# Kernel tuning notes

Hardware: AMD Instinct MI355X
Metric: run time of the kernel (lower is better)

The kernel has to match this reference:

```python
import jax, jax.numpy as jnp
import numpy as np

HIDDEN = 2048
NUM_HEADS = 16
HEAD_DIM = HIDDEN // NUM_HEADS  # 128
LAYER_IDX = 0


def setup_inputs() -> dict:
    key = jax.random.key(0)
    k1, k2, k3, k4, k5 = jax.random.split(key, 5)
    B, S = 2, 2048
    hidden_states = jax.random.normal(k1, (B, S, HIDDEN), dtype=jnp.float32)
    # causal mask, broadcastable to attn shape (B, Q, H, K)
    causal = jnp.tril(jnp.ones((S, S), dtype=jnp.bool_))  # [Q, K]
    attention_mask = causal[None, :, None, :]  # [1, Q, 1, K]
    c_attn_w = jax.random.normal(k2, (HIDDEN, HIDDEN + 2 * HEAD_DIM), dtype=jnp.float32) * 0.02
    c_attn_b = jax.random.normal(k3, (HIDDEN + 2 * HEAD_DIM,), dtype=jnp.float32) * 0.02
    c_proj_w = jax.random.normal(k4, (HIDDEN, HIDDEN), dtype=jnp.float32) * 0.02
    c_proj_b = jax.random.normal(k5, (HIDDEN,), dtype=jnp.float32) * 0.02
    return {
        "hidden_states": hidden_states,
        "attention_mask": attention_mask,
        "c_attn_w": c_attn_w,
        "c_attn_b": c_attn_b,
        "c_proj_w": c_proj_w,
        "c_proj_b": c_proj_b,
    }


def reference(hidden_states, attention_mask, c_attn_w, c_attn_b, c_proj_w, c_proj_b):
    B, S, D = hidden_states.shape
    H, hd = NUM_HEADS, HEAD_DIM
    # c_attn then split into per-head query and shared (MQA) key/value
    qkv = hidden_states @ c_attn_w + c_attn_b  # [B, S, D + 2*hd]
    query = qkv[..., :D].reshape(B, S, H, hd)  # [B, Q, H, hd]
    k = qkv[..., D:D + hd]                     # [B, K, hd] shared across heads
    v = qkv[..., D + hd:]                      # [B, K, hd]
    # fp32 input => upcast=False => unscale=1, scale = 1/sqrt(head_dim)
    scale = 1.0 / jnp.sqrt(jnp.float32(hd))
    scores = jnp.einsum('bqhd,bkd->bqhk', query, k) * scale  # [B, Q, H, K]
    mask_value = jnp.finfo(jnp.float32).min
    scores = jnp.where(attention_mask, scores, mask_value)
    attn = jax.nn.softmax(scores, axis=-1)
    attn_output = jnp.einsum('bqhk,bkd->bqhd', attn, v).reshape(B, S, D)
    attn_output = attn_output @ c_proj_w + c_proj_b
    return attn_output
```

## Files before the change

kernel.cpp:

```cpp
#include <hip/hip_runtime.h>
#include <hip/hip_bf16.h>

typedef __bf16 bf16_t;
typedef __bf16 bf16x8 __attribute__((ext_vector_type(8)));
typedef __bf16 bf16x4 __attribute__((ext_vector_type(4)));
typedef float f32x4 __attribute__((ext_vector_type(4)));

#define S_LEN 2048
#define HID   2048
#define NH    16
#define HD    128
#define QKVN  2304
#define NEG_BIG (-30000.0f)
#define RESCALE_THR 8.0f

__device__ __forceinline__ void gld_lds16(const bf16_t* g, bf16_t* l) {
  __builtin_amdgcn_global_load_lds(
      (const __attribute__((address_space(1))) void*)((const void*)g),
      (__attribute__((address_space(3))) void*)((void*)l), 16, 0, 0);
}

__global__ __launch_bounds__(256) void cvt_f32_bf16_kernel(
    const float* __restrict__ in, bf16_t* __restrict__ out, int n)
{
  int i = (blockIdx.x * 256 + threadIdx.x) * 4;
  if (i < n) {
    float4 v = *(const float4*)(in + i);
    bf16x4 o;
    o[0] = (bf16_t)v.x; o[1] = (bf16_t)v.y; o[2] = (bf16_t)v.z; o[3] = (bf16_t)v.w;
    *(bf16x4*)(out + i) = o;
  }
}

__global__ __launch_bounds__(256) void transpose_cvt_kernel(
    const float* __restrict__ in, bf16_t* __restrict__ out, int K, int N)
{
  int nc = threadIdx.x & 63;
  int kg = threadIdx.x >> 6;
  int n  = blockIdx.x * 64 + nc;
  int kb = blockIdx.y * 32 + kg * 8;
  bf16x8 v;
  #pragma unroll
  for (int i = 0; i < 8; ++i) v[i] = (bf16_t)in[(size_t)(kb + i) * N + n];
  *(bf16x8*)(out + (size_t)n * K + kb) = v;
}

__global__ __launch_bounds__(256) void vt_extract_kernel(
    const bf16_t* __restrict__ qkv, bf16_t* __restrict__ vtg)
{
  int d  = threadIdx.x & 127;
  int sg = threadIdx.x >> 7;
  int b  = blockIdx.y;
  int s8 = blockIdx.x * 2 + sg;
  bf16x8 v;
  #pragma unroll
  for (int i = 0; i < 8; ++i)
    v[i] = qkv[((size_t)(b * S_LEN + s8 * 8 + i)) * QKVN + HID + HD + d];
  *(bf16x8*)(vtg + ((size_t)(b * HD + d)) * S_LEN + s8 * 8) = v;
}

template <typename OutT>
__global__ __launch_bounds__(256) void gemm_bias_kernel(
    const bf16_t* __restrict__ A, const bf16_t* __restrict__ WT,
    const float* __restrict__ bias, OutT* __restrict__ C,
    int K, int lda, int ldc)
{
  __shared__ bf16_t Ash[128 * 64];
  __shared__ bf16_t Bsh[128 * 64];

  const int tid  = threadIdx.x;
  const int wave = tid >> 6;
  const int lane = tid & 63;
  const int quad = lane >> 4;
  const int c16  = lane & 15;
  const int wm = wave >> 1;
  const int wn = wave & 1;

  int id  = (int)(blockIdx.y * gridDim.x + blockIdx.x);
  int nwg = (int)(gridDim.x * gridDim.y);
  int swz = (nwg & 7) ? id : ((id & 7) * (nwg >> 3) + (id >> 3));
  const int n0 = (swz % (int)gridDim.x) * 128;
  const int m0 = (swz / (int)gridDim.x) * 128;

  f32x4 acc[4][4] = {};

  for (int k0 = 0; k0 < K; k0 += 64) {
    __syncthreads();
    #pragma unroll
    for (int j = 0; j < 4; ++j) {
      int cbase = wave * 256 + j * 64;
      int c = cbase + lane;
      int row = c >> 3;
      int kcl = (c ^ row) & 7;
      gld_lds16(A  + (size_t)(m0 + row) * lda + k0 + kcl * 8, Ash + cbase * 8);
      gld_lds16(WT + (size_t)(n0 + row) * K   + k0 + kcl * 8, Bsh + cbase * 8);
    }
    __syncthreads();

    #pragma unroll
    for (int kk = 0; kk < 2; ++kk) {
      bf16x8 af[4], bfr[4];
      #pragma unroll
      for (int rb = 0; rb < 4; ++rb) {
        int row = wm * 64 + rb * 16 + c16;
        int kcp = ((kk * 4 + quad) ^ row) & 7;
        af[rb] = *(const bf16x8*)(Ash + row * 64 + kcp * 8);
      }
      #pragma unroll
      for (int nt = 0; nt < 4; ++nt) {
        int row = wn * 64 + nt * 16 + c16;
        int kcp = ((kk * 4 + quad) ^ row) & 7;
        bfr[nt] = *(const bf16x8*)(Bsh + row * 64 + kcp * 8);
      }
      #pragma unroll
      for (int rb = 0; rb < 4; ++rb)
        #pragma unroll
        for (int nt = 0; nt < 4; ++nt)
          acc[rb][nt] = __builtin_amdgcn_mfma_f32_16x16x32_bf16(af[rb], bfr[nt],
                                                                acc[rb][nt], 0, 0, 0);
    }
  }

  #pragma unroll
  for (int nt = 0; nt < 4; ++nt) {
    int col = n0 + wn * 64 + nt * 16 + c16;
    float bv = bias[col];
    #pragma unroll
    for (int rb = 0; rb < 4; ++rb) {
      int rbase = m0 + wm * 64 + rb * 16 + quad * 4;
      #pragma unroll
      for (int r = 0; r < 4; ++r)
        C[(size_t)(rbase + r) * ldc + col] = (OutT)(acc[rb][nt][r] + bv);
    }
  }
}

__global__ __launch_bounds__(512, 4) void mqa_attn_kernel(
    const bf16_t* __restrict__ qkv, const bf16_t* __restrict__ vtg,
    bf16_t* __restrict__ out)
{
  __shared__ bf16_t Ksh[2][64 * 136];
  __shared__ bf16_t VTsh[2][128 * 72];

  const int tid  = threadIdx.x;
  const int wave = tid >> 6;
  const int g    = wave >> 2;
  const int wv   = wave & 3;
  const int lane = tid & 63;
  const int quad = lane >> 4;
  const int c16  = lane & 15;
  const int gt   = tid & 255;
  const int h = blockIdx.y;
  const int b = blockIdx.z;
  const float qscale = 0.08838834764831845f * 1.4426950408889634f;

  const bf16_t* kbase = qkv + (size_t)b * S_LEN * QKVN + HID;
  const bf16_t* vtb   = vtg + (size_t)b * HD * S_LEN;

  for (int half = 0; half < 2; ++half) {
    const int qb = half ? (31 - (int)blockIdx.x) : (int)blockIdx.x;
    const int q0 = qb * 64;
    const int qrow = q0 + wv * 16 + c16;

    const bf16_t* qp = qkv + ((size_t)(b * S_LEN + qrow)) * QKVN + h * HD;
    bf16x8 qf[4];
    #pragma unroll
    for (int ks = 0; ks < 4; ++ks) {
      bf16x8 t = *(const bf16x8*)(qp + ks * 32 + quad * 8);
      #pragma unroll
      for (int j = 0; j < 8; ++j) t[j] = (bf16_t)((float)t[j] * qscale);
      qf[ks] = t;
    }

    float m_q = NEG_BIG, l_q = 0.0f;
    f32x4 o[8] = {};
    const int nss = (qb + 2) >> 1;

    for (int ss = 0; ss < nss; ++ss) {
      const int kt = 2 * ss + g;
      const bool active = (kt <= qb);

      __syncthreads();
      if (active) {
        for (int c = gt; c < 1024; c += 256) {
          int key = c >> 4, dc = c & 15;
          *(bf16x8*)(&Ksh[g][key * 136 + dc * 8]) =
              *(const bf16x8*)(kbase + (size_t)(kt * 64 + key) * QKVN + dc * 8);
        }
        for (int c = gt; c < 1024; c += 256) {
          int d = c >> 3, kc = c & 7;
          *(bf16x8*)(&VTsh[g][d * 72 + kc * 8]) =
              *(const bf16x8*)(vtb + (size_t)d * S_LEN + kt * 64 + kc * 8);
        }
      }
      __syncthreads();

      float p[4][4];
      if (active) {
        f32x4 sacc[4] = {};
        __builtin_amdgcn_s_setprio(1);
        #pragma unroll
        for (int mt = 0; mt < 4; ++mt) {
          #pragma unroll
          for (int ks = 0; ks < 4; ++ks) {
            bf16x8 kf = *(const bf16x8*)(&Ksh[g][(mt * 16 + c16) * 136 + ks * 32 + quad * 8]);
            sacc[mt] = __builtin_amdgcn_mfma_f32_16x16x32_bf16(kf, qf[ks], sacc[mt], 0, 0, 0);
          }
        }
        __builtin_amdgcn_s_setprio(0);
        float mx = NEG_BIG;
        if (kt == qb) {
          #pragma unroll
          for (int mt = 0; mt < 4; ++mt) {
            #pragma unroll
            for (int r = 0; r < 4; ++r) {
              int key = kt * 64 + mt * 16 + quad * 4 + r;
              float v = sacc[mt][r];
              if (key > qrow) v = NEG_BIG;
              p[mt][r] = v;
              mx = fmaxf(mx, v);
            }
          }
        } else {
          #pragma unroll
          for (int mt = 0; mt < 4; ++mt) {
            #pragma unroll
            for (int r = 0; r < 4; ++r) {
              p[mt][r] = sacc[mt][r];
              mx = fmaxf(mx, sacc[mt][r]);
            }
          }
        }
        mx = fmaxf(mx, __shfl_xor(mx, 16));
        mx = fmaxf(mx, __shfl_xor(mx, 32));

        if (__any(mx > m_q + RESCALE_THR)) {
          float mn = fmaxf(m_q, mx);
          float alpha = __builtin_exp2f(m_q - mn);
          m_q = mn;
          l_q *= alpha;
          #pragma unroll
          for (int mt8 = 0; mt8 < 8; ++mt8) {
            #pragma unroll
            for (int r = 0; r < 4; ++r) o[mt8][r] *= alpha;
          }
        }

        float rs = 0.f;
        #pragma unroll
        for (int mt = 0; mt < 4; ++mt) {
          #pragma unroll
          for (int r = 0; r < 4; ++r) {
            float pe = __builtin_exp2f(p[mt][r] - m_q);
            p[mt][r] = pe;
            rs += pe;
          }
        }
        rs += __shfl_xor(rs, 16);
        rs += __shfl_xor(rs, 32);
        l_q += rs;
      }

      __syncthreads();
      if (active) {
        bf16_t* Pw = &Ksh[g][(wv * 16) * 136];
        #pragma unroll
        for (int mt = 0; mt < 4; ++mt) {
          bf16x4 pk;
          #pragma unroll
          for (int r = 0; r < 4; ++r) pk[r] = (bf16_t)p[mt][r];
          *(bf16x4*)(Pw + c16 * 136 + mt * 16 + quad * 4) = pk;
        }
        bf16x8 pf[2];
        #pragma unroll
        for (int kh = 0; kh < 2; ++kh)
          pf[kh] = *(const bf16x8*)(Pw + c16 * 136 + kh * 32 + quad * 8);
        __builtin_amdgcn_s_setprio(1);
        #pragma unroll
        for (int mt8 = 0; mt8 < 8; ++mt8) {
          #pragma unroll
          for (int kh = 0; kh < 2; ++kh) {
            bf16x8 vf = *(const bf16x8*)(&VTsh[g][(mt8 * 16 + c16) * 72 + kh * 32 + quad * 8]);
            o[mt8] = __builtin_amdgcn_mfma_f32_16x16x32_bf16(vf, pf[kh], o[mt8], 0, 0, 0);
          }
        }
        __builtin_amdgcn_s_setprio(0);
      }
    }

    __syncthreads();
    float* scr = (float*)&VTsh[0][0];
    float* mls = scr + 4 * 16 * 132;
    if (g == 1) {
      float* op = scr + (wv * 16 + c16) * 132;
      #pragma unroll
      for (int mt8 = 0; mt8 < 8; ++mt8)
        *(f32x4*)(op + mt8 * 16 + quad * 4) = o[mt8];
      if (quad == 0) {
        mls[wv * 32 + c16] = m_q;
        mls[wv * 32 + 16 + c16] = l_q;
      }
    }
    __syncthreads();
    if (g == 0) {
      float m1 = mls[wv * 32 + c16];
      float l1 = mls[wv * 32 + 16 + c16];
      float mF = fmaxf(m_q, m1);
      float a0 = __builtin_exp2f(m_q - mF);
      float a1 = __builtin_exp2f(m1 - mF);
      float inv = 1.0f / fmaxf(a0 * l_q + a1 * l1, 1e-20f);
      a0 *= inv; a1 *= inv;
      const float* op = scr + (wv * 16 + c16) * 132;
      bf16_t* Osh = &Ksh[0][(wv * 16) * 136];
      #pragma unroll
      for (int mt8 = 0; mt8 < 8; ++mt8) {
        f32x4 o1 = *(const f32x4*)(op + mt8 * 16 + quad * 4);
        bf16x4 pk;
        #pragma unroll
        for (int r = 0; r < 4; ++r) pk[r] = (bf16_t)(o[mt8][r] * a0 + o1[r] * a1);
        *(bf16x4*)(Osh + c16 * 136 + mt8 * 16 + quad * 4) = pk;
      }
      int ql = lane >> 2, dc = lane & 3;
      #pragma unroll
      for (int i = 0; i < 4; ++i) {
        bf16x8 v = *(const bf16x8*)(Osh + ql * 136 + dc * 8 + i * 32);
        *(bf16x8*)(out + ((size_t)(b * S_LEN + q0 + wv * 16 + ql)) * HID
                       + h * HD + dc * 8 + i * 32) = v;
      }
    }
  }
}

extern "C" void kernel_launch(void* const* d_in, const int* in_sizes, int n_in,
                              void* d_out, int out_size, void* d_ws, size_t ws_size,
                              hipStream_t stream) {
  const float* hidden_f   = (const float*)d_in[0];
  const float* c_attn_w_f = (const float*)d_in[2];
  const float* c_attn_b_f = (const float*)d_in[3];
  const float* c_proj_w_f = (const float*)d_in[4];
  const float* c_proj_b_f = (const float*)d_in[5];
  float* out = (float*)d_out;

  const int M = 2 * S_LEN;
  const int nH  = M * HID;
  const int nWq = HID * QKVN;
  const int nWp = HID * HID;

  bf16_t* hbf   = (bf16_t*)d_ws;
  bf16_t* wqT   = hbf  + nH;
  bf16_t* wpT   = wqT  + nWq;
  bf16_t* qkv   = wpT  + nWp;
  bf16_t* attn  = qkv  + (size_t)M * QKVN;
  bf16_t* vtg   = attn + (size_t)M * HID;

  cvt_f32_bf16_kernel<<<nH / 1024, 256, 0, stream>>>(hidden_f, hbf, nH);
  dim3 gt1(QKVN / 64, HID / 32);
  transpose_cvt_kernel<<<gt1, 256, 0, stream>>>(c_attn_w_f, wqT, HID, QKVN);
  dim3 gt2(HID / 64, HID / 32);
  transpose_cvt_kernel<<<gt2, 256, 0, stream>>>(c_proj_w_f, wpT, HID, HID);

  dim3 g1(QKVN / 128, M / 128);
  gemm_bias_kernel<bf16_t><<<g1, 256, 0, stream>>>(hbf, wqT, c_attn_b_f, qkv,
                                                   HID, HID, QKVN);

  dim3 gv(S_LEN / 16, 2);
  vt_extract_kernel<<<gv, 256, 0, stream>>>(qkv, vtg);

  dim3 g2(16, NH, 2);
  mqa_attn_kernel<<<g2, 512, 0, stream>>>(qkv, vtg, attn);

  dim3 g3(HID / 128, M / 128);
  gemm_bias_kernel<float><<<g3, 256, 0, stream>>>(attn, wpT, c_proj_b_f, out,
                                                  HID, HID, HID);
}
```

Measured before the change: 338.0 us.

## Restructure MQA attention to 128-row query tiles with swizzled P buffer

The attention kernel now gives each block one 128-row query tile, with each of the 8 waves owning 16 rows. This replaces the old scheme of two wave groups splitting KV tiles and merging partial softmax states at the end. Each K/V tile loaded into LDS is shared by twice as many queries, which removes the cross-group merge and one set of shared buffers. The P staging area uses an XOR swizzle to cut LDS bank conflicts, and the query-block mapping is rotated by head and batch to balance causal work across blocks. Waves whose rows lie entirely before a KV tile skip compute, but they still hit every barrier.

```diff
diff --git a/kernel.cpp b/kernel.cpp
--- a/kernel.cpp
+++ b/kernel.cpp
@@ -139,17 +139,15 @@
     const bf16_t* __restrict__ qkv, const bf16_t* __restrict__ vtg,
     bf16_t* __restrict__ out)
 {
-  __shared__ bf16_t Ksh[2][64 * 136];
-  __shared__ bf16_t VTsh[2][128 * 72];
+  __shared__ bf16_t sh[17920];
+  bf16_t* Ksh  = sh;
+  bf16_t* VTsh = sh + 64 * 136;
 
   const int tid  = threadIdx.x;
-  const int wave = tid >> 6;
-  const int g    = wave >> 2;
-  const int wv   = wave & 3;
+  const int wv   = tid >> 6;
   const int lane = tid & 63;
   const int quad = lane >> 4;
   const int c16  = lane & 15;
-  const int gt   = tid & 255;
   const int h = blockIdx.y;
   const int b = blockIdx.z;
   const float qscale = 0.08838834764831845f * 1.4426950408889634f;
@@ -157,177 +155,160 @@
   const bf16_t* kbase = qkv + (size_t)b * S_LEN * QKVN + HID;
   const bf16_t* vtb   = vtg + (size_t)b * HD * S_LEN;
 
-  for (int half = 0; half < 2; ++half) {
-    const int qb = half ? (31 - (int)blockIdx.x) : (int)blockIdx.x;
-    const int q0 = qb * 64;
-    const int qrow = q0 + wv * 16 + c16;
-
-    const bf16_t* qp = qkv + ((size_t)(b * S_LEN + qrow)) * QKVN + h * HD;
-    bf16x8 qf[4];
-    #pragma unroll
-    for (int ks = 0; ks < 4; ++ks) {
-      bf16x8 t = *(const bf16x8*)(qp + ks * 32 + quad * 8);
-      #pragma unroll
-      for (int j = 0; j < 8; ++j) t[j] = (bf16_t)((float)t[j] * qscale);
-      qf[ks] = t;
-    }
-
-    float m_q = NEG_BIG, l_q = 0.0f;
-    f32x4 o[8] = {};
-    const int nss = (qb + 2) >> 1;
-
-    for (int ss = 0; ss < nss; ++ss) {
-      const int kt = 2 * ss + g;
-      const bool active = (kt <= qb);
-
-      __syncthreads();
-      if (active) {
-        for (int c = gt; c < 1024; c += 256) {
-          int key = c >> 4, dc = c & 15;
-          *(bf16x8*)(&Ksh[g][key * 136 + dc * 8]) =
-              *(const bf16x8*)(kbase + (size_t)(kt * 64 + key) * QKVN + dc * 8);
-        }
-        for (int c = gt; c < 1024; c += 256) {
-          int d = c >> 3, kc = c & 7;
-          *(bf16x8*)(&VTsh[g][d * 72 + kc * 8]) =
-              *(const bf16x8*)(vtb + (size_t)d * S_LEN + kt * 64 + kc * 8);
-        }
-      }
-      __syncthreads();
-
-      float p[4][4];
-      if (active) {
-        f32x4 sacc[4] = {};
-        __builtin_amdgcn_s_setprio(1);
-        #pragma unroll
-        for (int mt = 0; mt < 4; ++mt) {
-          #pragma unroll
-          for (int ks = 0; ks < 4; ++ks) {
-            bf16x8 kf = *(const bf16x8*)(&Ksh[g][(mt * 16 + c16) * 136 + ks * 32 + quad * 8]);
-            sacc[mt] = __builtin_amdgcn_mfma_f32_16x16x32_bf16(kf, qf[ks], sacc[mt], 0, 0, 0);
-          }
-        }
-        __builtin_amdgcn_s_setprio(0);
-        float mx = NEG_BIG;
-        if (kt == qb) {
-          #pragma unroll
-          for (int mt = 0; mt < 4; ++mt) {
-            #pragma unroll
-            for (int r = 0; r < 4; ++r) {
-              int key = kt * 64 + mt * 16 + quad * 4 + r;
-              float v = sacc[mt][r];
-              if (key > qrow) v = NEG_BIG;
-              p[mt][r] = v;
-              mx = fmaxf(mx, v);
-            }
-          }
-        } else {
-          #pragma unroll
-          for (int mt = 0; mt < 4; ++mt) {
-            #pragma unroll
-            for (int r = 0; r < 4; ++r) {
-              p[mt][r] = sacc[mt][r];
-              mx = fmaxf(mx, sacc[mt][r]);
-            }
-          }
-        }
-        mx = fmaxf(mx, __shfl_xor(mx, 16));
-        mx = fmaxf(mx, __shfl_xor(mx, 32));
-
-        if (__any(mx > m_q + RESCALE_THR)) {
-          float mn = fmaxf(m_q, mx);
-          float alpha = __builtin_exp2f(m_q - mn);
-          m_q = mn;
-          l_q *= alpha;
-          #pragma unroll
-          for (int mt8 = 0; mt8 < 8; ++mt8) {
-            #pragma unroll
-            for (int r = 0; r < 4; ++r) o[mt8][r] *= alpha;
-          }
-        }
-
-        float rs = 0.f;
+  const int qh = ((int)blockIdx.x + h) & 15;
+  const int Q  = b ? (15 - qh) : qh;
+  const int q0 = Q * 128;
+  const int qrow = q0 + wv * 16 + c16;
+  const int ntile = 2 * Q + 2;
+
+  const bf16_t* qp = qkv + ((size_t)(b * S_LEN + qrow)) * QKVN + h * HD;
+  bf16x8 qf[4];
+  #pragma unroll
+  for (int ks = 0; ks < 4; ++ks) {
+    bf16x8 t = *(const bf16x8*)(qp + ks * 32 + quad * 8);
+    #pragma unroll
+    for (int j = 0; j < 8; ++j) t[j] = (bf16_t)((float)t[j] * qscale);
+    qf[ks] = t;
+  }
+
+  float m_q = NEG_BIG, l_q = 0.0f;
+  f32x4 o[8] = {};
+
+  const int prow = wv * 16 + c16;
+  bf16_t* Pbase = sh + (size_t)prow * 64;
+  const int rsw = prow & 7;
+
+  for (int kt = 0; kt < ntile; ++kt) {
+    __syncthreads();
+    {
+      const bf16_t* kb = kbase + (size_t)kt * 64 * QKVN;
+      const bf16_t* vb = vtb + kt * 64;
+      #pragma unroll
+      for (int i = 0; i < 2; ++i) {
+        int c = tid + i * 512;
+        int key = c >> 4, dc = (c & 15) * 8;
+        *(bf16x8*)(&Ksh[key * 136 + dc]) =
+            *(const bf16x8*)(kb + (size_t)key * QKVN + dc);
+      }
+      #pragma unroll
+      for (int i = 0; i < 2; ++i) {
+        int c = tid + i * 512;
+        int d = c >> 3, kc = (c & 7) * 8;
+        *(bf16x8*)(&VTsh[d * 72 + kc]) =
+            *(const bf16x8*)(vb + (size_t)d * S_LEN + kc);
+      }
+    }
+    __syncthreads();
+
+    const bool wactive = (kt * 64) <= (q0 + wv * 16 + 15);
+    f32x4 sacc[4] = {};
+    if (wactive) {
+      __builtin_amdgcn_s_setprio(1);
+      #pragma unroll
+      for (int mt = 0; mt < 4; ++mt) {
+        #pragma unroll
+        for (int ks = 0; ks < 4; ++ks) {
+          bf16x8 kf = *(const bf16x8*)(&Ksh[(mt * 16 + c16) * 136 + ks * 32 + quad * 8]);
+          sacc[mt] = __builtin_amdgcn_mfma_f32_16x16x32_bf16(kf, qf[ks], sacc[mt], 0, 0, 0);
+        }
+      }
+      __builtin_amdgcn_s_setprio(0);
+
+      float mx = NEG_BIG;
+      if (kt * 64 + 63 > q0 + wv * 16) {
         #pragma unroll
         for (int mt = 0; mt < 4; ++mt) {
           #pragma unroll
           for (int r = 0; r < 4; ++r) {
-            float pe = __builtin_exp2f(p[mt][r] - m_q);
-            p[mt][r] = pe;
-            rs += pe;
+            int key = kt * 64 + mt * 16 + quad * 4 + r;
+            float v = sacc[mt][r];
+            if (key > qrow) v = NEG_BIG;
+            sacc[mt][r] = v;
+            mx = fmaxf(mx, v);
           }
         }
-        rs += __shfl_xor(rs, 16);
-        rs += __shfl_xor(rs, 32);
-        l_q += rs;
-      }
-
-      __syncthreads();
-      if (active) {
-        bf16_t* Pw = &Ksh[g][(wv * 16) * 136];
+      } else {
         #pragma unroll
         for (int mt = 0; mt < 4; ++mt) {
-          bf16x4 pk;
           #pragma unroll
-          for (int r = 0; r < 4; ++r) pk[r] = (bf16_t)p[mt][r];
-          *(bf16x4*)(Pw + c16 * 136 + mt * 16 + quad * 4) = pk;
-        }
-        bf16x8 pf[2];
-        #pragma unroll
-        for (int kh = 0; kh < 2; ++kh)
-          pf[kh] = *(const bf16x8*)(Pw + c16 * 136 + kh * 32 + quad * 8);
-        __builtin_amdgcn_s_setprio(1);
+          for (int r = 0; r < 4; ++r) mx = fmaxf(mx, sacc[mt][r]);
+        }
+      }
+      mx = fmaxf(mx, __shfl_xor(mx, 16));
+      mx = fmaxf(mx, __shfl_xor(mx, 32));
+
+      if (__any(mx > m_q + RESCALE_THR)) {
+        float mn = fmaxf(m_q, mx);
+        float alpha = __builtin_exp2f(m_q - mn);
+        m_q = mn;
+        l_q *= alpha;
         #pragma unroll
         for (int mt8 = 0; mt8 < 8; ++mt8) {
           #pragma unroll
-          for (int kh = 0; kh < 2; ++kh) {
-            bf16x8 vf = *(const bf16x8*)(&VTsh[g][(mt8 * 16 + c16) * 72 + kh * 32 + quad * 8]);
-            o[mt8] = __builtin_amdgcn_mfma_f32_16x16x32_bf16(vf, pf[kh], o[mt8], 0, 0, 0);
-          }
-        }
-        __builtin_amdgcn_s_setprio(0);
-      }
-    }
-
-    __syncthreads();
-    float* scr = (float*)&VTsh[0][0];
-    float* mls = scr + 4 * 16 * 132;
-    if (g == 1) {
-      float* op = scr + (wv * 16 + c16) * 132;
-      #pragma unroll
-      for (int mt8 = 0; mt8 < 8; ++mt8)
-        *(f32x4*)(op + mt8 * 16 + quad * 4) = o[mt8];
-      if (quad == 0) {
-        mls[wv * 32 + c16] = m_q;
-        mls[wv * 32 + 16 + c16] = l_q;
-      }
-    }
-    __syncthreads();
-    if (g == 0) {
-      float m1 = mls[wv * 32 + c16];
-      float l1 = mls[wv * 32 + 16 + c16];
-      float mF = fmaxf(m_q, m1);
-      float a0 = __builtin_exp2f(m_q - mF);
-      float a1 = __builtin_exp2f(m1 - mF);
-      float inv = 1.0f / fmaxf(a0 * l_q + a1 * l1, 1e-20f);
-      a0 *= inv; a1 *= inv;
-      const float* op = scr + (wv * 16 + c16) * 132;
-      bf16_t* Osh = &Ksh[0][(wv * 16) * 136];
+          for (int r = 0; r < 4; ++r) o[mt8][r] *= alpha;
+        }
+      }
+
+      float rs = 0.f;
+      #pragma unroll
+      for (int mt = 0; mt < 4; ++mt) {
+        #pragma unroll
+        for (int r = 0; r < 4; ++r) {
+          float pe = __builtin_exp2f(sacc[mt][r] - m_q);
+          sacc[mt][r] = pe;
+          rs += pe;
+        }
+      }
+      rs += __shfl_xor(rs, 16);
+      rs += __shfl_xor(rs, 32);
+      l_q += rs;
+    }
+
+    __syncthreads();
+    if (wactive) {
+      #pragma unroll
+      for (int mt = 0; mt < 4; ++mt) {
+        bf16x4 pk;
+        #pragma unroll
+        for (int r = 0; r < 4; ++r) pk[r] = (bf16_t)sacc[mt][r];
+        int ch = 2 * mt + (quad >> 1);
+        *(bf16x4*)(Pbase + (((ch ^ rsw) << 3) + (quad & 1) * 4)) = pk;
+      }
+      bf16x8 pf[2];
+      #pragma unroll
+      for (int kh = 0; kh < 2; ++kh) {
+        int ch = 4 * kh + quad;
+        pf[kh] = *(const bf16x8*)(Pbase + ((ch ^ rsw) << 3));
+      }
+      __builtin_amdgcn_s_setprio(1);
       #pragma unroll
       for (int mt8 = 0; mt8 < 8; ++mt8) {
-        f32x4 o1 = *(const f32x4*)(op + mt8 * 16 + quad * 4);
-        bf16x4 pk;
-        #pragma unroll
-        for (int r = 0; r < 4; ++r) pk[r] = (bf16_t)(o[mt8][r] * a0 + o1[r] * a1);
-        *(bf16x4*)(Osh + c16 * 136 + mt8 * 16 + quad * 4) = pk;
-      }
-      int ql = lane >> 2, dc = lane & 3;
-      #pragma unroll
-      for (int i = 0; i < 4; ++i) {
-        bf16x8 v = *(const bf16x8*)(Osh + ql * 136 + dc * 8 + i * 32);
-        *(bf16x8*)(out + ((size_t)(b * S_LEN + q0 + wv * 16 + ql)) * HID
-                       + h * HD + dc * 8 + i * 32) = v;
-      }
-    }
+        #pragma unroll
+        for (int kh = 0; kh < 2; ++kh) {
+          bf16x8 vf = *(const bf16x8*)(&VTsh[(mt8 * 16 + c16) * 72 + kh * 32 + quad * 8]);
+          o[mt8] = __builtin_amdgcn_mfma_f32_16x16x32_bf16(vf, pf[kh], o[mt8], 0, 0, 0);
+        }
+      }
+      __builtin_amdgcn_s_setprio(0);
+    }
+  }
+
+  __syncthreads();
+  float inv = 1.0f / fmaxf(l_q, 1e-20f);
+  bf16_t* Osh = sh;
+  #pragma unroll
+  for (int mt8 = 0; mt8 < 8; ++mt8) {
+    bf16x4 pk;
+    #pragma unroll
+    for (int r = 0; r < 4; ++r) pk[r] = (bf16_t)(o[mt8][r] * inv);
+    *(bf16x4*)(&Osh[(size_t)prow * 136 + mt8 * 16 + quad * 4]) = pk;
+  }
+  int ql = lane >> 2, dc = lane & 3;
+  #pragma unroll
+  for (int i = 0; i < 4; ++i) {
+    bf16x8 v = *(const bf16x8*)(&Osh[(size_t)(wv * 16 + ql) * 136 + dc * 8 + i * 32]);
+    *(bf16x8*)(out + ((size_t)(b * S_LEN + q0 + wv * 16 + ql)) * HID
+                   + h * HD + dc * 8 + i * 32) = v;
   }
 }
 
```

New measurement: 333.6 us. Within noise of the previous version (-1.3%).
